# Kernel optimization log

Measured on AMD Instinct MI355X. Metric: run time of the kernel, lower is better.

The kernel has to match this reference:

```python
import jax, jax.numpy as jnp
import numpy as np

B, F, E = 2048, 24, 128
P = F * (F - 1) // 2  # 276 upper-triangular field pairs


def setup_inputs() -> dict:
    key = jax.random.key(0)
    k1, k2 = jax.random.split(key)
    x = jax.random.normal(k1, (B, F, E), dtype=jnp.float32)
    # keras random_normal initializer uses small stddev; 0.05 mirrors that
    kernel = jax.random.normal(k2, (E, P, E), dtype=jnp.float32) * 0.05
    return {"x": x, "kernel": kernel}


def reference(x, kernel):
    F_ = x.shape[1]
    p_idx, q_idx = np.triu_indices(F_, k=1)  # static pair index lists (i < j)
    Xp = x[:, p_idx, :]  # [B, P, E]
    Xq = x[:, q_idx, :]  # [B, P, E]
    # result[b,p] = sum_{d,e} Xp[b,p,e] * kernel[d,p,e] * Xq[b,p,d]
    # fused einsum avoids the [B, E, P, E] intermediate the TF code materializes
    result = jnp.einsum("bpe,dpe,bpd->bp", Xp, kernel, Xq)
    return result
```

## Files before the change

kernel.cpp:

```cpp
#include <hip/hip_runtime.h>
#include <stdint.h>

#define B_SZ 2048
#define F_SZ 24
#define E_SZ 128
#define P_SZ 276
#define BT   256
#define NWG  (P_SZ * 8)

#define XT_ELEMS (B_SZ * F_SZ * E_SZ)
#define KB_ELEMS (P_SZ * E_SZ * E_SZ)
#define WS_NEED  ((size_t)(XT_ELEMS + KB_ELEMS) * 2)

#define XPREP_BLKS (F_SZ * 64)
#define KPREP_BLKS (KB_ELEMS / 2048)

typedef __bf16 bf16x8 __attribute__((ext_vector_type(8)));
typedef __bf16 bf16x4 __attribute__((ext_vector_type(4)));
typedef float  f32x16 __attribute__((ext_vector_type(16)));

__global__ __launch_bounds__(256) void prepack_all(
    const float* __restrict__ x, const float* __restrict__ kern,
    __bf16* __restrict__ xft, __bf16* __restrict__ kb)
{
    const int bid = blockIdx.x;
    const int tid = threadIdx.x;
    if (bid < XPREP_BLKS) {
        const int f = bid >> 6, grp = bid & 63;
        const float* srcb = x + ((size_t)grp * 32 * F_SZ + f) * E_SZ;
        __bf16* dst = xft + (size_t)(f * 64 + grp) * 4096;
#pragma unroll
        for (int u = 0; u < 2; ++u) {
            const int s = tid * 2 + u;
            const int row = s & 31;
            const int e0  = (s >> 6) * 16 + ((s >> 5) & 1) * 8;
            const float* src = srcb + (size_t)row * (F_SZ * E_SZ) + e0;
            float4 v0 = *(const float4*)src;
            float4 v1 = *(const float4*)(src + 4);
            bf16x8 h;
            h[0] = (__bf16)v0.x; h[1] = (__bf16)v0.y; h[2] = (__bf16)v0.z; h[3] = (__bf16)v0.w;
            h[4] = (__bf16)v1.x; h[5] = (__bf16)v1.y; h[6] = (__bf16)v1.z; h[7] = (__bf16)v1.w;
            *(bf16x8*)(dst + s * 8) = h;
        }
    } else {
        int g = (bid - XPREP_BLKS) * 256 + tid;
        int p = g >> 11, r = g & 2047;
        int d = r >> 4, s = r & 15;
        const float* src = kern + ((size_t)d * P_SZ + p) * E_SZ + ((s ^ (d & 15)) << 3);
        float4 v0 = *(const float4*)src;
        float4 v1 = *(const float4*)(src + 4);
        bf16x8 h;
        h[0] = (__bf16)v0.x; h[1] = (__bf16)v0.y; h[2] = (__bf16)v0.z; h[3] = (__bf16)v0.w;
        h[4] = (__bf16)v1.x; h[5] = (__bf16)v1.y; h[6] = (__bf16)v1.z; h[7] = (__bf16)v1.w;
        *(bf16x8*)(kb + (size_t)g * 8) = h;
    }
}

__global__ __launch_bounds__(512, 4) void opn_main(
    const __bf16* __restrict__ xft, const __bf16* __restrict__ kb,
    float* __restrict__ out)
{
    __shared__ short sK[E_SZ * E_SZ];

    const int tid = threadIdx.x, w = tid >> 6, lane = tid & 63;
    const int l31 = lane & 31, hi = lane >> 5;
    const int orig = blockIdx.x;
    const int bb = orig & 7;
    const int p  = orig >> 3;

    int fp = 0, rem = p;
    while (rem >= F_SZ - 1 - fp) { rem -= F_SZ - 1 - fp; ++fp; }
    const int fq = fp + 1 + rem;

    const __bf16* kp = kb + (size_t)p * (E_SZ * E_SZ);
#pragma unroll
    for (int t = 0; t < 4; ++t) {
        const int base = (w * 4 + t) * 64;
        __builtin_amdgcn_global_load_lds(
            (const __attribute__((address_space(1))) void*)(kp + (size_t)(base + lane) * 8),
            (__attribute__((address_space(3))) void*)(&sK[base * 8]),
            16, 0, 2 );
    }

    const int grp = bb * 8 + w;
    bf16x8 xpf[8];
    const __bf16* xpb = xft + (size_t)(fp * 64 + grp) * 4096 + lane * 8;
#pragma unroll
    for (int kk = 0; kk < 8; ++kk)
        xpf[kk] = *(const bf16x8*)(xpb + kk * 512);
    bf16x4 xqr[4][4];
    const __bf16* xqb = xft + (size_t)(fq * 64 + grp) * 4096 + l31 * 8 + hi * 4;
#pragma unroll
    for (int mt = 0; mt < 4; ++mt)
#pragma unroll
        for (int q = 0; q < 4; ++q)
            xqr[mt][q] = *(const bf16x4*)(xqb + (mt * 2 + (q >> 1)) * 512 + (q & 1) * 256);

    __syncthreads();

    float s0 = 0.f, s1 = 0.f;
#pragma unroll
    for (int mt = 0; mt < 4; ++mt) {
        f32x16 acc;
#pragma unroll
        for (int q = 0; q < 16; ++q) acc[q] = 0.f;
        const int arow = mt * 32 + l31;
        const short* kRow = &sK[arow * E_SZ];
        const int asw = (arow & 15) << 3;
#pragma unroll
        for (int kk = 0; kk < 8; ++kk) {
            bf16x8 afr = *(const bf16x8*)&kRow[((kk * 2 + hi) << 3) ^ asw];
            acc = __builtin_amdgcn_mfma_f32_32x32x16_bf16(afr, xpf[kk], acc, 0, 0, 0);
        }
#pragma unroll
        for (int q = 0; q < 4; ++q) {
            const bf16x4 xq = xqr[mt][q];
            s0 += acc[q * 4 + 0] * (float)xq[0] + acc[q * 4 + 1] * (float)xq[1];
            s1 += acc[q * 4 + 2] * (float)xq[2] + acc[q * 4 + 3] * (float)xq[3];
        }
    }
    float s = s0 + s1;
    s += __shfl_xor(s, 32);
    if (hi == 0)
        out[(size_t)(grp * 32 + l31) * P_SZ + p] = s;
}

__global__ __launch_bounds__(512, 4) void opn_fallback(
    const float* __restrict__ x, const float* __restrict__ kern,
    float* __restrict__ out)
{
    __shared__ short sA[128 * E_SZ];
    __shared__ short sB[E_SZ * E_SZ];
    __shared__ float red[2][128];

    const int tid = threadIdx.x;
    const int orig = blockIdx.x;
    const int nwg2 = P_SZ * 16;
    const int wgid = (orig & 7) * (nwg2 / 8) + (orig >> 3);
    const int p  = wgid >> 4;
    const int bb = wgid & 15;
    const int b0 = bb * 128;

    int fp = 0, rem = p;
    while (rem >= F_SZ - 1 - fp) { rem -= F_SZ - 1 - fp; ++fp; }
    const int fq = fp + 1 + rem;

#pragma unroll
    for (int k = 0; k < 4; ++k) {
        int i = tid + k * 512;
        int r = i >> 4, s8 = i & 15;
        const float* src = x + ((size_t)(b0 + r) * F_SZ + fp) * E_SZ + s8 * 8;
        float4 v0 = *(const float4*)src;
        float4 v1 = *(const float4*)(src + 4);
        bf16x8 h;
        h[0] = (__bf16)v0.x; h[1] = (__bf16)v0.y; h[2] = (__bf16)v0.z; h[3] = (__bf16)v0.w;
        h[4] = (__bf16)v1.x; h[5] = (__bf16)v1.y; h[6] = (__bf16)v1.z; h[7] = (__bf16)v1.w;
        *(bf16x8*)&sA[r * E_SZ + ((s8 ^ (r & 15)) << 3)] = h;
    }
#pragma unroll
    for (int k = 0; k < 4; ++k) {
        int i = tid + k * 512;
        int r = i >> 4, s8 = i & 15;
        const float* src = kern + ((size_t)r * P_SZ + p) * E_SZ + s8 * 8;
        float4 v0 = *(const float4*)src;
        float4 v1 = *(const float4*)(src + 4);
        bf16x8 h;
        h[0] = (__bf16)v0.x; h[1] = (__bf16)v0.y; h[2] = (__bf16)v0.z; h[3] = (__bf16)v0.w;
        h[4] = (__bf16)v1.x; h[5] = (__bf16)v1.y; h[6] = (__bf16)v1.z; h[7] = (__bf16)v1.w;
        *(bf16x8*)&sB[r * E_SZ + ((s8 ^ (r & 15)) << 3)] = h;
    }
    __syncthreads();

    const int w = tid >> 6, lane = tid & 63;
    const int l31 = lane & 31, hi = lane >> 5;
    const int mh = w >> 2, ng = w & 3;

    f32x16 acc[2];
#pragma unroll
    for (int mt = 0; mt < 2; ++mt)
#pragma unroll
        for (int j = 0; j < 16; ++j) acc[mt][j] = 0.f;

    const int brow = ng * 32 + l31;
#pragma unroll
    for (int kk = 0; kk < 8; ++kk) {
        const int e8 = kk * 2 + hi;
        bf16x8 bfr = *(const bf16x8*)&sA[brow * E_SZ + ((e8 ^ (brow & 15)) << 3)];
#pragma unroll
        for (int mt = 0; mt < 2; ++mt) {
            int arow = (mh * 2 + mt) * 32 + l31;
            bf16x8 afr = *(const bf16x8*)&sB[arow * E_SZ + ((e8 ^ (arow & 15)) << 3)];
            acc[mt] = __builtin_amdgcn_mfma_f32_32x32x16_bf16(afr, bfr, acc[mt], 0, 0, 0);
        }
    }

    const float* xqp = x + ((size_t)(b0 + brow) * F_SZ + fq) * E_SZ;
    float sv = 0.f;
#pragma unroll
    for (int mt = 0; mt < 2; ++mt) {
        const int dbase = (mh * 2 + mt) * 32 + hi * 4;
#pragma unroll
        for (int q = 0; q < 4; ++q) {
            float4 xq = *(const float4*)(xqp + dbase + q * 8);
            sv += acc[mt][q * 4 + 0] * xq.x + acc[mt][q * 4 + 1] * xq.y
                + acc[mt][q * 4 + 2] * xq.z + acc[mt][q * 4 + 3] * xq.w;
        }
    }
    sv += __shfl_xor(sv, 32);
    if (hi == 0) red[mh][brow] = sv;
    __syncthreads();

    if (tid < 128)
        out[(size_t)(b0 + tid) * P_SZ + p] = red[0][tid] + red[1][tid];
}

extern "C" void kernel_launch(void* const* d_in, const int* in_sizes, int n_in,
                              void* d_out, int out_size, void* d_ws, size_t ws_size,
                              hipStream_t stream) {
    const float* x    = (const float*)d_in[0];
    const float* kern = (const float*)d_in[1];
    float* out = (float*)d_out;

    if (ws_size >= WS_NEED) {
        __bf16* xft = (__bf16*)d_ws;
        __bf16* kb  = xft + XT_ELEMS;
        prepack_all<<<dim3(XPREP_BLKS + KPREP_BLKS), 256, 0, stream>>>(x, kern, xft, kb);
        opn_main<<<dim3(NWG), 512, 0, stream>>>(xft, kb, out);
    } else {
        opn_fallback<<<dim3(P_SZ * 16), 512, 0, stream>>>(x, kern, out);
    }
}
```

Before: 49.59 us.

## Group pairs by shared q-field and double-buffer kernel tiles across pairs

The main kernel now gives each workgroup a segment of up to four pairs that share the same q field. The xq fragments load once per segment, and the per-pair kernel slices stream into two LDS buffers while the previous pair computes, using explicit vmcnt waits and barriers. The x prepack now stages rows through a padded shared tile so global reads are contiguous. This cuts the grid from 2208 to 624 workgroups and doubles LDS per block, which may lower occupancy and load balance in exchange for overlap and fewer redundant loads.

After: 115.9 us. +133.7%, slower.

```diff
diff --git a/kernel.cpp b/kernel.cpp
--- a/kernel.cpp
+++ b/kernel.cpp
@@ -6,7 +6,9 @@
 #define E_SZ 128
 #define P_SZ 276
 #define BT   256
-#define NWG  (P_SZ * 8)
+#define SEGLEN 4
+#define NSEG 78
+#define NWG  (NSEG * 8)
 
 #define XT_ELEMS (B_SZ * F_SZ * E_SZ)
 #define KB_ELEMS (P_SZ * E_SZ * E_SZ)
@@ -27,19 +29,30 @@
     const int tid = threadIdx.x;
     if (bid < XPREP_BLKS) {
         const int f = bid >> 6, grp = bid & 63;
-        const float* srcb = x + ((size_t)grp * 32 * F_SZ + f) * E_SZ;
+        __shared__ float sT[32][129];
+        {
+            const int row = tid >> 3, c0 = (tid & 7) * 16;
+            const float* src = x + ((size_t)(grp * 32 + row) * F_SZ + f) * E_SZ + c0;
+            float4 v0 = ((const float4*)src)[0];
+            float4 v1 = ((const float4*)src)[1];
+            float4 v2 = ((const float4*)src)[2];
+            float4 v3 = ((const float4*)src)[3];
+            *(float4*)&sT[row][c0]      = v0;
+            *(float4*)&sT[row][c0 + 4]  = v1;
+            *(float4*)&sT[row][c0 + 8]  = v2;
+            *(float4*)&sT[row][c0 + 12] = v3;
+        }
+        __syncthreads();
         __bf16* dst = xft + (size_t)(f * 64 + grp) * 4096;
 #pragma unroll
         for (int u = 0; u < 2; ++u) {
             const int s = tid * 2 + u;
             const int row = s & 31;
             const int e0  = (s >> 6) * 16 + ((s >> 5) & 1) * 8;
-            const float* src = srcb + (size_t)row * (F_SZ * E_SZ) + e0;
-            float4 v0 = *(const float4*)src;
-            float4 v1 = *(const float4*)(src + 4);
             bf16x8 h;
-            h[0] = (__bf16)v0.x; h[1] = (__bf16)v0.y; h[2] = (__bf16)v0.z; h[3] = (__bf16)v0.w;
-            h[4] = (__bf16)v1.x; h[5] = (__bf16)v1.y; h[6] = (__bf16)v1.z; h[7] = (__bf16)v1.w;
+#pragma unroll
+            for (int i = 0; i < 8; ++i)
+                h[i] = (__bf16)sT[row][e0 + i];
             *(bf16x8*)(dst + s * 8) = h;
         }
     } else {
@@ -56,73 +69,105 @@
     }
 }
 
+#define COMPUTE_PAIR(KBUF, XP, PJ)                                            \
+  {                                                                           \
+    float s0_ = 0.f, s1_ = 0.f;                                               \
+    _Pragma("unroll")                                                         \
+    for (int mt = 0; mt < 4; ++mt) {                                          \
+      f32x16 acc;                                                             \
+      _Pragma("unroll")                                                       \
+      for (int q = 0; q < 16; ++q) acc[q] = 0.f;                              \
+      const int arow_ = mt * 32 + l31;                                        \
+      const short* kRow_ = &(KBUF)[arow_ * E_SZ];                             \
+      const int asw_ = (arow_ & 15) << 3;                                     \
+      _Pragma("unroll")                                                       \
+      for (int kk = 0; kk < 8; ++kk) {                                        \
+        bf16x8 afr_ = *(const bf16x8*)&kRow_[((kk * 2 + hi) << 3) ^ asw_];    \
+        acc = __builtin_amdgcn_mfma_f32_32x32x16_bf16(afr_, (XP)[kk], acc,    \
+                                                      0, 0, 0);               \
+      }                                                                       \
+      _Pragma("unroll")                                                       \
+      for (int q = 0; q < 4; ++q) {                                           \
+        const bf16x4 xq_ = xqr[mt][q];                                        \
+        s0_ += acc[q*4+0]*(float)xq_[0] + acc[q*4+1]*(float)xq_[1];           \
+        s1_ += acc[q*4+2]*(float)xq_[2] + acc[q*4+3]*(float)xq_[3];           \
+      }                                                                       \
+    }                                                                         \
+    float sv_ = s0_ + s1_;                                                    \
+    sv_ += __shfl_xor(sv_, 32);                                               \
+    if (hi == 0) out[(size_t)(grp * 32 + l31) * P_SZ + (PJ)] = sv_;           \
+  }
+
 __global__ __launch_bounds__(512, 4) void opn_main(
     const __bf16* __restrict__ xft, const __bf16* __restrict__ kb,
     float* __restrict__ out)
 {
-    __shared__ short sK[E_SZ * E_SZ];
+    __shared__ short sK0[E_SZ * E_SZ];
+    __shared__ short sK1[E_SZ * E_SZ];
 
     const int tid = threadIdx.x, w = tid >> 6, lane = tid & 63;
     const int l31 = lane & 31, hi = lane >> 5;
     const int orig = blockIdx.x;
     const int bb = orig & 7;
-    const int p  = orig >> 3;
-
-    int fp = 0, rem = p;
-    while (rem >= F_SZ - 1 - fp) { rem -= F_SZ - 1 - fp; ++fp; }
-    const int fq = fp + 1 + rem;
-
-    const __bf16* kp = kb + (size_t)p * (E_SZ * E_SZ);
-#pragma unroll
-    for (int t = 0; t < 4; ++t) {
-        const int base = (w * 4 + t) * 64;
-        __builtin_amdgcn_global_load_lds(
-            (const __attribute__((address_space(1))) void*)(kp + (size_t)(base + lane) * 8),
-            (__attribute__((address_space(3))) void*)(&sK[base * 8]),
-            16, 0, 2 );
-    }
+    const int il = orig >> 3;
+
+    int s = il, fq = 23;
+    for (;;) { int ns = (fq + 3) >> 2; if (s < ns) break; s -= ns; --fq; }
+    const int q0  = s * SEGLEN;
+    const int len = (fq - q0 < SEGLEN) ? (fq - q0) : SEGLEN;
 
     const int grp = bb * 8 + w;
-    bf16x8 xpf[8];
-    const __bf16* xpb = xft + (size_t)(fp * 64 + grp) * 4096 + lane * 8;
-#pragma unroll
-    for (int kk = 0; kk < 8; ++kk)
-        xpf[kk] = *(const bf16x8*)(xpb + kk * 512);
+
+    auto pOf = [&](int fp) { return fp * 23 - (fp * (fp - 1)) / 2 + (fq - fp - 1); };
+
+    auto stage_k = [&](short* dst, int p) {
+        const __bf16* kp = kb + (size_t)p * (E_SZ * E_SZ);
+#pragma unroll
+        for (int t = 0; t < 4; ++t) {
+            const int base = (w * 4 + t) * 64;
+            __builtin_amdgcn_global_load_lds(
+                (const __attribute__((address_space(1))) void*)(kp + (size_t)(base + lane) * 8),
+                (__attribute__((address_space(3))) void*)(&dst[base * 8]),
+                16, 0, 0);
+        }
+    };
+    auto load_xp = [&](bf16x8* xp, int fp) {
+        const __bf16* xpb = xft + (size_t)(fp * 64 + grp) * 4096 + lane * 8;
+#pragma unroll
+        for (int kk = 0; kk < 8; ++kk)
+            xp[kk] = *(const bf16x8*)(xpb + kk * 512);
+    };
+
     bf16x4 xqr[4][4];
-    const __bf16* xqb = xft + (size_t)(fq * 64 + grp) * 4096 + l31 * 8 + hi * 4;
-#pragma unroll
-    for (int mt = 0; mt < 4; ++mt)
-#pragma unroll
-        for (int q = 0; q < 4; ++q)
-            xqr[mt][q] = *(const bf16x4*)(xqb + (mt * 2 + (q >> 1)) * 512 + (q & 1) * 256);
-
-    __syncthreads();
-
-    float s0 = 0.f, s1 = 0.f;
-#pragma unroll
-    for (int mt = 0; mt < 4; ++mt) {
-        f32x16 acc;
-#pragma unroll
-        for (int q = 0; q < 16; ++q) acc[q] = 0.f;
-        const int arow = mt * 32 + l31;
-        const short* kRow = &sK[arow * E_SZ];
-        const int asw = (arow & 15) << 3;
-#pragma unroll
-        for (int kk = 0; kk < 8; ++kk) {
-            bf16x8 afr = *(const bf16x8*)&kRow[((kk * 2 + hi) << 3) ^ asw];
-            acc = __builtin_amdgcn_mfma_f32_32x32x16_bf16(afr, xpf[kk], acc, 0, 0, 0);
-        }
-#pragma unroll
-        for (int q = 0; q < 4; ++q) {
-            const bf16x4 xq = xqr[mt][q];
-            s0 += acc[q * 4 + 0] * (float)xq[0] + acc[q * 4 + 1] * (float)xq[1];
-            s1 += acc[q * 4 + 2] * (float)xq[2] + acc[q * 4 + 3] * (float)xq[3];
-        }
-    }
-    float s = s0 + s1;
-    s += __shfl_xor(s, 32);
-    if (hi == 0)
-        out[(size_t)(grp * 32 + l31) * P_SZ + p] = s;
+    {
+        const __bf16* xqb = xft + (size_t)(fq * 64 + grp) * 4096 + l31 * 8 + hi * 4;
+#pragma unroll
+        for (int mt = 0; mt < 4; ++mt)
+#pragma unroll
+            for (int q = 0; q < 4; ++q)
+                xqr[mt][q] = *(const bf16x4*)(xqb + (mt * 2 + (q >> 1)) * 512 + (q & 1) * 256);
+    }
+
+    bf16x8 xpA[8], xpB[8];
+    stage_k(sK0, pOf(q0));
+    load_xp(xpA, q0);
+
+#pragma unroll
+    for (int j = 0; j < SEGLEN; ++j) {
+        if (j >= len) break;
+        if (j + 1 < len) {
+            if ((j + 1) & 1) { stage_k(sK1, pOf(q0 + j + 1)); load_xp(xpB, q0 + j + 1); }
+            else             { stage_k(sK0, pOf(q0 + j + 1)); load_xp(xpA, q0 + j + 1); }
+            asm volatile("s_waitcnt vmcnt(12)" ::: "memory");
+        } else {
+            asm volatile("s_waitcnt vmcnt(0)" ::: "memory");
+        }
+        __builtin_amdgcn_sched_barrier(0);
+        __builtin_amdgcn_s_barrier();
+        if (j & 1) COMPUTE_PAIR(sK1, xpB, pOf(q0 + j))
+        else       COMPUTE_PAIR(sK0, xpA, pOf(q0 + j))
+        __builtin_amdgcn_s_barrier();
+    }
 }
 
 __global__ __launch_bounds__(512, 4) void opn_fallback(
```

## Prepack kernel into MFMA fragment order and read it directly to registers

Applied to the files above, without the earlier changes.

The prepack kernel now stages 32x128 tiles of x and the kernel weights through padded shared memory, so global reads are coalesced and the bf16 output is written in the exact per-lane MFMA fragment order. The main kernel drops its shared-memory staging of the per-pair kernel matrix and the block barrier, and instead loads A fragments straight from global memory into registers for each 32-row tile. This removes LDS traffic and a sync from the main kernel, at the cost of more global loads per wave (every wave reloads the full 128x128 kernel slice, relying on cache) and higher register pressure, with the occupancy hint removed from launch bounds.

Measured after the change: 56.81 us. 14.6% more time.

```diff
diff --git a/kernel.cpp b/kernel.cpp
--- a/kernel.cpp
+++ b/kernel.cpp
@@ -5,7 +5,6 @@
 #define F_SZ 24
 #define E_SZ 128
 #define P_SZ 276
-#define BT   256
 #define NWG  (P_SZ * 8)
 
 #define XT_ELEMS (B_SZ * F_SZ * E_SZ)
@@ -13,7 +12,7 @@
 #define WS_NEED  ((size_t)(XT_ELEMS + KB_ELEMS) * 2)
 
 #define XPREP_BLKS (F_SZ * 64)
-#define KPREP_BLKS (KB_ELEMS / 2048)
+#define KPREP_BLKS (P_SZ * 4)
 
 typedef __bf16 bf16x8 __attribute__((ext_vector_type(8)));
 typedef __bf16 bf16x4 __attribute__((ext_vector_type(4)));
@@ -21,47 +20,73 @@
 
 __global__ __launch_bounds__(256) void prepack_all(
     const float* __restrict__ x, const float* __restrict__ kern,
-    __bf16* __restrict__ xft, __bf16* __restrict__ kb)
+    __bf16* __restrict__ xft, __bf16* __restrict__ kbf)
 {
     const int bid = blockIdx.x;
     const int tid = threadIdx.x;
+    __shared__ float sT[32][129];
     if (bid < XPREP_BLKS) {
         const int f = bid >> 6, grp = bid & 63;
-        const float* srcb = x + ((size_t)grp * 32 * F_SZ + f) * E_SZ;
+        {
+            const int row = tid >> 3, c0 = (tid & 7) * 16;
+            const float* src = x + ((size_t)(grp * 32 + row) * F_SZ + f) * E_SZ + c0;
+            float4 v0 = ((const float4*)src)[0];
+            float4 v1 = ((const float4*)src)[1];
+            float4 v2 = ((const float4*)src)[2];
+            float4 v3 = ((const float4*)src)[3];
+            *(float4*)&sT[row][c0]      = v0;
+            *(float4*)&sT[row][c0 + 4]  = v1;
+            *(float4*)&sT[row][c0 + 8]  = v2;
+            *(float4*)&sT[row][c0 + 12] = v3;
+        }
+        __syncthreads();
         __bf16* dst = xft + (size_t)(f * 64 + grp) * 4096;
 #pragma unroll
         for (int u = 0; u < 2; ++u) {
             const int s = tid * 2 + u;
             const int row = s & 31;
             const int e0  = (s >> 6) * 16 + ((s >> 5) & 1) * 8;
-            const float* src = srcb + (size_t)row * (F_SZ * E_SZ) + e0;
-            float4 v0 = *(const float4*)src;
-            float4 v1 = *(const float4*)(src + 4);
             bf16x8 h;
-            h[0] = (__bf16)v0.x; h[1] = (__bf16)v0.y; h[2] = (__bf16)v0.z; h[3] = (__bf16)v0.w;
-            h[4] = (__bf16)v1.x; h[5] = (__bf16)v1.y; h[6] = (__bf16)v1.z; h[7] = (__bf16)v1.w;
+#pragma unroll
+            for (int i = 0; i < 8; ++i)
+                h[i] = (__bf16)sT[row][e0 + i];
             *(bf16x8*)(dst + s * 8) = h;
         }
     } else {
-        int g = (bid - XPREP_BLKS) * 256 + tid;
-        int p = g >> 11, r = g & 2047;
-        int d = r >> 4, s = r & 15;
-        const float* src = kern + ((size_t)d * P_SZ + p) * E_SZ + ((s ^ (d & 15)) << 3);
-        float4 v0 = *(const float4*)src;
-        float4 v1 = *(const float4*)(src + 4);
-        bf16x8 h;
-        h[0] = (__bf16)v0.x; h[1] = (__bf16)v0.y; h[2] = (__bf16)v0.z; h[3] = (__bf16)v0.w;
-        h[4] = (__bf16)v1.x; h[5] = (__bf16)v1.y; h[6] = (__bf16)v1.z; h[7] = (__bf16)v1.w;
-        *(bf16x8*)(kb + (size_t)g * 8) = h;
-    }
-}
-
-__global__ __launch_bounds__(512, 4) void opn_main(
-    const __bf16* __restrict__ xft, const __bf16* __restrict__ kb,
+        const int kb = bid - XPREP_BLKS;
+        const int p = kb >> 2, mt = kb & 3;
+        {
+            const int row = tid >> 3, c0 = (tid & 7) * 16;
+            const float* src = kern + ((size_t)(mt * 32 + row) * P_SZ + p) * E_SZ + c0;
+            float4 v0 = ((const float4*)src)[0];
+            float4 v1 = ((const float4*)src)[1];
+            float4 v2 = ((const float4*)src)[2];
+            float4 v3 = ((const float4*)src)[3];
+            *(float4*)&sT[row][c0]      = v0;
+            *(float4*)&sT[row][c0 + 4]  = v1;
+            *(float4*)&sT[row][c0 + 8]  = v2;
+            *(float4*)&sT[row][c0 + 12] = v3;
+        }
+        __syncthreads();
+        __bf16* dst = kbf + (size_t)p * 16384 + mt * 4096;
+#pragma unroll
+        for (int u = 0; u < 2; ++u) {
+            const int s = tid * 2 + u;
+            const int lane = s & 63, l31 = lane & 31, hi2 = lane >> 5;
+            const int e0 = (s >> 6) * 16 + hi2 * 8;
+            bf16x8 h;
+#pragma unroll
+            for (int i = 0; i < 8; ++i)
+                h[i] = (__bf16)sT[l31][e0 + i];
+            *(bf16x8*)(dst + s * 8) = h;
+        }
+    }
+}
+
+__global__ __launch_bounds__(512) void opn_main(
+    const __bf16* __restrict__ xft, const __bf16* __restrict__ kbf,
     float* __restrict__ out)
 {
-    __shared__ short sK[E_SZ * E_SZ];
-
     const int tid = threadIdx.x, w = tid >> 6, lane = tid & 63;
     const int l31 = lane & 31, hi = lane >> 5;
     const int orig = blockIdx.x;
@@ -72,22 +97,14 @@
     while (rem >= F_SZ - 1 - fp) { rem -= F_SZ - 1 - fp; ++fp; }
     const int fq = fp + 1 + rem;
 
-    const __bf16* kp = kb + (size_t)p * (E_SZ * E_SZ);
-#pragma unroll
-    for (int t = 0; t < 4; ++t) {
-        const int base = (w * 4 + t) * 64;
-        __builtin_amdgcn_global_load_lds(
-            (const __attribute__((address_space(1))) void*)(kp + (size_t)(base + lane) * 8),
-            (__attribute__((address_space(3))) void*)(&sK[base * 8]),
-            16, 0, 2 );
-    }
-
     const int grp = bb * 8 + w;
+
     bf16x8 xpf[8];
     const __bf16* xpb = xft + (size_t)(fp * 64 + grp) * 4096 + lane * 8;
 #pragma unroll
     for (int kk = 0; kk < 8; ++kk)
         xpf[kk] = *(const bf16x8*)(xpb + kk * 512);
+
     bf16x4 xqr[4][4];
     const __bf16* xqb = xft + (size_t)(fq * 64 + grp) * 4096 + l31 * 8 + hi * 4;
 #pragma unroll
@@ -96,22 +113,20 @@
         for (int q = 0; q < 4; ++q)
             xqr[mt][q] = *(const bf16x4*)(xqb + (mt * 2 + (q >> 1)) * 512 + (q & 1) * 256);
 
-    __syncthreads();
-
+    const __bf16* kpb = kbf + (size_t)p * 16384 + lane * 8;
     float s0 = 0.f, s1 = 0.f;
 #pragma unroll
     for (int mt = 0; mt < 4; ++mt) {
+        bf16x8 kf[8];
+#pragma unroll
+        for (int kk = 0; kk < 8; ++kk)
+            kf[kk] = *(const bf16x8*)(kpb + (mt * 8 + kk) * 512);
         f32x16 acc;
 #pragma unroll
         for (int q = 0; q < 16; ++q) acc[q] = 0.f;
-        const int arow = mt * 32 + l31;
-        const short* kRow = &sK[arow * E_SZ];
-        const int asw = (arow & 15) << 3;
-#pragma unroll
-        for (int kk = 0; kk < 8; ++kk) {
-            bf16x8 afr = *(const bf16x8*)&kRow[((kk * 2 + hi) << 3) ^ asw];
-            acc = __builtin_amdgcn_mfma_f32_32x32x16_bf16(afr, xpf[kk], acc, 0, 0, 0);
-        }
+#pragma unroll
+        for (int kk = 0; kk < 8; ++kk)
+            acc = __builtin_amdgcn_mfma_f32_32x32x16_bf16(kf[kk], xpf[kk], acc, 0, 0, 0);
 #pragma unroll
         for (int q = 0; q < 4; ++q) {
             const bf16x4 xq = xqr[mt][q];
@@ -223,9 +238,9 @@
 
     if (ws_size >= WS_NEED) {
         __bf16* xft = (__bf16*)d_ws;
-        __bf16* kb  = xft + XT_ELEMS;
-        prepack_all<<<dim3(XPREP_BLKS + KPREP_BLKS), 256, 0, stream>>>(x, kern, xft, kb);
-        opn_main<<<dim3(NWG), 512, 0, stream>>>(xft, kb, out);
+        __bf16* kbf = xft + XT_ELEMS;
+        prepack_all<<<dim3(XPREP_BLKS + KPREP_BLKS), 256, 0, stream>>>(x, kern, xft, kbf);
+        opn_main<<<dim3(NWG), 512, 0, stream>>>(xft, kbf, out);
     } else {
         opn_fallback<<<dim3(P_SZ * 16), 512, 0, stream>>>(x, kern, out);
     }
```

## Hold kernel fragments in registers across batch groups and stage x transpose via LDS

Applied to the files above, without the earlier changes.

The main kernel now runs 256 threads per workgroup instead of 512. Each wave keeps its half of the pair's kernel matrix in registers and loops over four batch groups, so the LDS reads of K are reused across groups. Partial sums from the two d-halves are combined through a shared reduction buffer, and output is written with one coalesced store per thread. The prepack step now reads x rows with contiguous float4 loads into a padded LDS tile before converting to bf16, which is meant to make the global reads coalesced. In exchange the main kernel uses more registers, has fewer threads per block, and processes its batch groups serially inside each wave.

Measured after the change: 51.67 us. 1.04x slower.

```diff
diff --git a/kernel.cpp b/kernel.cpp
--- a/kernel.cpp
+++ b/kernel.cpp
@@ -27,19 +27,30 @@
     const int tid = threadIdx.x;
     if (bid < XPREP_BLKS) {
         const int f = bid >> 6, grp = bid & 63;
-        const float* srcb = x + ((size_t)grp * 32 * F_SZ + f) * E_SZ;
+        __shared__ float sT[32][129];
+        {
+            const int row = tid >> 3, c0 = (tid & 7) * 16;
+            const float* src = x + ((size_t)(grp * 32 + row) * F_SZ + f) * E_SZ + c0;
+            float4 v0 = ((const float4*)src)[0];
+            float4 v1 = ((const float4*)src)[1];
+            float4 v2 = ((const float4*)src)[2];
+            float4 v3 = ((const float4*)src)[3];
+            *(float4*)&sT[row][c0]      = v0;
+            *(float4*)&sT[row][c0 + 4]  = v1;
+            *(float4*)&sT[row][c0 + 8]  = v2;
+            *(float4*)&sT[row][c0 + 12] = v3;
+        }
+        __syncthreads();
         __bf16* dst = xft + (size_t)(f * 64 + grp) * 4096;
 #pragma unroll
         for (int u = 0; u < 2; ++u) {
             const int s = tid * 2 + u;
             const int row = s & 31;
             const int e0  = (s >> 6) * 16 + ((s >> 5) & 1) * 8;
-            const float* src = srcb + (size_t)row * (F_SZ * E_SZ) + e0;
-            float4 v0 = *(const float4*)src;
-            float4 v1 = *(const float4*)(src + 4);
             bf16x8 h;
-            h[0] = (__bf16)v0.x; h[1] = (__bf16)v0.y; h[2] = (__bf16)v0.z; h[3] = (__bf16)v0.w;
-            h[4] = (__bf16)v1.x; h[5] = (__bf16)v1.y; h[6] = (__bf16)v1.z; h[7] = (__bf16)v1.w;
+#pragma unroll
+            for (int i = 0; i < 8; ++i)
+                h[i] = (__bf16)sT[row][e0 + i];
             *(bf16x8*)(dst + s * 8) = h;
         }
     } else {
@@ -56,11 +67,12 @@
     }
 }
 
-__global__ __launch_bounds__(512, 4) void opn_main(
+__global__ __launch_bounds__(256, 4) void opn_main(
     const __bf16* __restrict__ xft, const __bf16* __restrict__ kb,
     float* __restrict__ out)
 {
     __shared__ short sK[E_SZ * E_SZ];
+    __shared__ float red[2][BT];
 
     const int tid = threadIdx.x, w = tid >> 6, lane = tid & 63;
     const int l31 = lane & 31, hi = lane >> 5;
@@ -74,55 +86,70 @@
 
     const __bf16* kp = kb + (size_t)p * (E_SZ * E_SZ);
 #pragma unroll
-    for (int t = 0; t < 4; ++t) {
-        const int base = (w * 4 + t) * 64;
+    for (int t = 0; t < 8; ++t) {
+        const int base = (w * 8 + t) * 64;
         __builtin_amdgcn_global_load_lds(
             (const __attribute__((address_space(1))) void*)(kp + (size_t)(base + lane) * 8),
             (__attribute__((address_space(3))) void*)(&sK[base * 8]),
-            16, 0, 2 );
-    }
-
-    const int grp = bb * 8 + w;
-    bf16x8 xpf[8];
-    const __bf16* xpb = xft + (size_t)(fp * 64 + grp) * 4096 + lane * 8;
-#pragma unroll
-    for (int kk = 0; kk < 8; ++kk)
-        xpf[kk] = *(const bf16x8*)(xpb + kk * 512);
-    bf16x4 xqr[4][4];
-    const __bf16* xqb = xft + (size_t)(fq * 64 + grp) * 4096 + l31 * 8 + hi * 4;
-#pragma unroll
-    for (int mt = 0; mt < 4; ++mt)
-#pragma unroll
-        for (int q = 0; q < 4; ++q)
-            xqr[mt][q] = *(const bf16x4*)(xqb + (mt * 2 + (q >> 1)) * 512 + (q & 1) * 256);
-
-    __syncthreads();
-
-    float s0 = 0.f, s1 = 0.f;
-#pragma unroll
-    for (int mt = 0; mt < 4; ++mt) {
-        f32x16 acc;
-#pragma unroll
-        for (int q = 0; q < 16; ++q) acc[q] = 0.f;
-        const int arow = mt * 32 + l31;
+            16, 0, 0);
+    }
+    __syncthreads();
+
+    const int dhalf = w >> 1;
+    bf16x8 kf[2][8];
+#pragma unroll
+    for (int mtl = 0; mtl < 2; ++mtl) {
+        const int arow = (dhalf * 2 + mtl) * 32 + l31;
         const short* kRow = &sK[arow * E_SZ];
         const int asw = (arow & 15) << 3;
 #pragma unroll
-        for (int kk = 0; kk < 8; ++kk) {
-            bf16x8 afr = *(const bf16x8*)&kRow[((kk * 2 + hi) << 3) ^ asw];
-            acc = __builtin_amdgcn_mfma_f32_32x32x16_bf16(afr, xpf[kk], acc, 0, 0, 0);
-        }
-#pragma unroll
-        for (int q = 0; q < 4; ++q) {
-            const bf16x4 xq = xqr[mt][q];
-            s0 += acc[q * 4 + 0] * (float)xq[0] + acc[q * 4 + 1] * (float)xq[1];
-            s1 += acc[q * 4 + 2] * (float)xq[2] + acc[q * 4 + 3] * (float)xq[3];
-        }
-    }
-    float s = s0 + s1;
-    s += __shfl_xor(s, 32);
-    if (hi == 0)
-        out[(size_t)(grp * 32 + l31) * P_SZ + p] = s;
+        for (int kk = 0; kk < 8; ++kk)
+            kf[mtl][kk] = *(const bf16x8*)&kRow[((kk * 2 + hi) << 3) ^ asw];
+    }
+
+#pragma unroll 1
+    for (int j = 0; j < 4; ++j) {
+        const int g   = (w & 1) * 4 + j;
+        const int grp = bb * 8 + g;
+
+        bf16x8 xpf[8];
+        const __bf16* xpb = xft + (size_t)(fp * 64 + grp) * 4096 + lane * 8;
+#pragma unroll
+        for (int kk = 0; kk < 8; ++kk)
+            xpf[kk] = *(const bf16x8*)(xpb + kk * 512);
+
+        const __bf16* xqb = xft + (size_t)(fq * 64 + grp) * 4096 + l31 * 8 + hi * 4;
+
+        float s0 = 0.f, s1 = 0.f;
+#pragma unroll
+        for (int mtl = 0; mtl < 2; ++mtl) {
+            const int mt = dhalf * 2 + mtl;
+            bf16x4 xq0 = *(const bf16x4*)(xqb + (mt * 2 + 0) * 512 + 0);
+            bf16x4 xq1 = *(const bf16x4*)(xqb + (mt * 2 + 0) * 512 + 256);
+            bf16x4 xq2 = *(const bf16x4*)(xqb + (mt * 2 + 1) * 512 + 0);
+            bf16x4 xq3 = *(const bf16x4*)(xqb + (mt * 2 + 1) * 512 + 256);
+            f32x16 acc;
+#pragma unroll
+            for (int q = 0; q < 16; ++q) acc[q] = 0.f;
+#pragma unroll
+            for (int kk = 0; kk < 8; ++kk)
+                acc = __builtin_amdgcn_mfma_f32_32x32x16_bf16(kf[mtl][kk], xpf[kk], acc, 0, 0, 0);
+            s0 += acc[ 0] * (float)xq0[0] + acc[ 1] * (float)xq0[1]
+                + acc[ 2] * (float)xq0[2] + acc[ 3] * (float)xq0[3];
+            s1 += acc[ 4] * (float)xq1[0] + acc[ 5] * (float)xq1[1]
+                + acc[ 6] * (float)xq1[2] + acc[ 7] * (float)xq1[3];
+            s0 += acc[ 8] * (float)xq2[0] + acc[ 9] * (float)xq2[1]
+                + acc[10] * (float)xq2[2] + acc[11] * (float)xq2[3];
+            s1 += acc[12] * (float)xq3[0] + acc[13] * (float)xq3[1]
+                + acc[14] * (float)xq3[2] + acc[15] * (float)xq3[3];
+        }
+        float s = s0 + s1;
+        s += __shfl_xor(s, 32);
+        if (hi == 0) red[dhalf][g * 32 + l31] = s;
+    }
+    __syncthreads();
+
+    out[(size_t)(bb * BT + tid) * P_SZ + p] = red[0][tid] + red[1][tid];
 }
 
 __global__ __launch_bounds__(512, 4) void opn_fallback(
@@ -152,10 +179,10 @@
         const float* src = x + ((size_t)(b0 + r) * F_SZ + fp) * E_SZ + s8 * 8;
         float4 v0 = *(const float4*)src;
         float4 v1 = *(const float4*)(src + 4);
-        bf16x8 h;
-        h[0] = (__bf16)v0.x; h[1] = (__bf16)v0.y; h[2] = (__bf16)v0.z; h[3] = (__bf16)v0.w;
-        h[4] = (__bf16)v1.x; h[5] = (__bf16)v1.y; h[6] = (__bf16)v1.z; h[7] = (__bf16)v1.w;
-        *(bf16x8*)&sA[r * E_SZ + ((s8 ^ (r & 15)) << 3)] = h;
+        bf16x8 hh;
+        hh[0] = (__bf16)v0.x; hh[1] = (__bf16)v0.y; hh[2] = (__bf16)v0.z; hh[3] = (__bf16)v0.w;
+        hh[4] = (__bf16)v1.x; hh[5] = (__bf16)v1.y; hh[6] = (__bf16)v1.z; hh[7] = (__bf16)v1.w;
+        *(bf16x8*)&sA[r * E_SZ + ((s8 ^ (r & 15)) << 3)] = hh;
     }
 #pragma unroll
     for (int k = 0; k < 4; ++k) {
@@ -164,10 +191,10 @@
         const float* src = kern + ((size_t)r * P_SZ + p) * E_SZ + s8 * 8;
         float4 v0 = *(const float4*)src;
         float4 v1 = *(const float4*)(src + 4);
-        bf16x8 h;
-        h[0] = (__bf16)v0.x; h[1] = (__bf16)v0.y; h[2] = (__bf16)v0.z; h[3] = (__bf16)v0.w;
-        h[4] = (__bf16)v1.x; h[5] = (__bf16)v1.y; h[6] = (__bf16)v1.z; h[7] = (__bf16)v1.w;
-        *(bf16x8*)&sB[r * E_SZ + ((s8 ^ (r & 15)) << 3)] = h;
+        bf16x8 hh;
+        hh[0] = (__bf16)v0.x; hh[1] = (__bf16)v0.y; hh[2] = (__bf16)v0.z; hh[3] = (__bf16)v0.w;
+        hh[4] = (__bf16)v1.x; hh[5] = (__bf16)v1.y; hh[6] = (__bf16)v1.z; hh[7] = (__bf16)v1.w;
+        *(bf16x8*)&sB[r * E_SZ + ((s8 ^ (r & 15)) << 3)] = hh;
     }
     __syncthreads();
 
@@ -225,7 +252,7 @@
         __bf16* xft = (__bf16*)d_ws;
         __bf16* kb  = xft + XT_ELEMS;
         prepack_all<<<dim3(XPREP_BLKS + KPREP_BLKS), 256, 0, stream>>>(x, kern, xft, kb);
-        opn_main<<<dim3(NWG), 512, 0, stream>>>(xft, kb, out);
+        opn_main<<<dim3(NWG), 256, 0, stream>>>(xft, kb, out);
     } else {
         opn_fallback<<<dim3(P_SZ * 16), 512, 0, stream>>>(x, kern, out);
     }
```
